# Optimization experiments

Measured on AMD Instinct MI355X. Metric: run time of the kernel, lower is better.

Reference implementation:

```python
import jax, jax.numpy as jnp
import numpy as np

N = 100000   # nodes
E = 1600000  # edges
D = 128      # input = hidden channels
L = 4        # 1 + num_convs GIN layers
G = 512      # graphs in batch
BN_EPS = 1e-5


def setup_inputs() -> dict:
    key = jax.random.key(0)
    ks = jax.random.split(key, 10)
    s = 1.0 / np.sqrt(D)
    x = jax.random.normal(ks[0], (N, D), jnp.float32)
    edge_index = jax.random.randint(ks[1], (2, E), 0, N)
    batch = jnp.sort(jax.random.randint(ks[2], (N,), 0, G))
    return {
        "x": x,
        "edge_index": edge_index,
        "batch": batch,
        "W1": jax.random.normal(ks[3], (L, D, D), jnp.float32) * s,
        "b1": jnp.zeros((L, D), jnp.float32),
        "gamma": jnp.ones((L, D), jnp.float32),
        "beta": jnp.zeros((L, D), jnp.float32),
        "W2": jax.random.normal(ks[4], (L, D, D), jnp.float32) * s,
        "b2": jnp.zeros((L, D), jnp.float32),
        "lin_W": jax.random.normal(ks[5], (D, 2), jnp.float32) * s,
        "lin_b": jnp.zeros((2,), jnp.float32),
    }


def reference(x, edge_index, batch, W1, b1, gamma, beta, W2, b2, lin_W, lin_b):
    src, dst = edge_index[0], edge_index[1]
    h = x
    for l in range(L):
        # GINConv, eps=0: (1+eps)*x_i + sum_{j->i} x_j  (scatter-add over edges)
        agg = jax.ops.segment_sum(h[src], dst, num_segments=N)  # [N, D]
        z = h + agg
        # MLP: Linear -> BatchNorm1d (training stats) -> ELU -> Linear -> ELU
        z = z @ W1[l] + b1[l]
        mu = jnp.mean(z, axis=0)
        var = jnp.mean((z - mu) ** 2, axis=0)  # biased var, as torch BN
        z = (z - mu) * jax.lax.rsqrt(var + BN_EPS) * gamma[l] + beta[l]
        z = jax.nn.elu(z)
        h = jax.nn.elu(z @ W2[l] + b2[l])
    # global_mean_pool: per-graph segment mean
    sums = jax.ops.segment_sum(h, batch, num_segments=G)             # [G, D]
    cnt = jax.ops.segment_sum(jnp.ones((N, 1), h.dtype), batch, num_segments=G)
    pooled = sums / jnp.maximum(cnt, 1.0)
    return pooled @ lin_W + lin_b  # [G, 2]
```

## Files before the change

kernel.cpp:

```cpp
#include <hip/hip_runtime.h>
#include <cstdint>

#define D 128
#define BKT_SHIFT 8
#define BKT_CAP 5120
#define EDGES_PER_BLOCK 4096
#define NREP 8

typedef __attribute__((ext_vector_type(4))) float floatx4;
typedef __attribute__((ext_vector_type(4))) _Float16 half4;
typedef __attribute__((ext_vector_type(8))) _Float16 half8;

__device__ __forceinline__ float elu_f(float x) {
    return x > 0.0f ? x : __expf(x) - 1.0f;
}

__global__ void init_cursor_kernel(int* __restrict__ gcursor, int NB) {
    int t = blockIdx.x * 256 + threadIdx.x;
    if (t < NB) gcursor[t] = t * BKT_CAP;
}

__global__ __launch_bounds__(256) void bucket_scatter_kernel(
    const int* __restrict__ src, const int* __restrict__ dst,
    int* __restrict__ gcursor, int2* __restrict__ staging, int E, int NB) {
    __shared__ int lcnt[512];
    __shared__ int lbase[512];
    int t = threadIdx.x;
    lcnt[t] = 0; lcnt[t + 256] = 0;
    __syncthreads();
    int base = blockIdx.x * EDGES_PER_BLOCK;
    int s_[16], d_[16], r_[16];
#pragma unroll
    for (int i = 0; i < 16; ++i) {
        int idx = base + i * 256 + t;
        if (idx < E) {
            s_[i] = src[idx];
            d_[i] = dst[idx];
            r_[i] = atomicAdd(&lcnt[d_[i] >> BKT_SHIFT], 1);
        }
    }
    __syncthreads();
    for (int b = t; b < NB; b += 256) {
        int c = lcnt[b];
        if (c) lbase[b] = atomicAdd(&gcursor[b], c);
    }
    __syncthreads();
#pragma unroll
    for (int i = 0; i < 16; ++i) {
        int idx = base + i * 256 + t;
        if (idx < E) {
            int bkt = d_[i] >> BKT_SHIFT;
            staging[lbase[bkt] + r_[i]] = make_int2(s_[i], d_[i]);
        }
    }
}

__global__ __launch_bounds__(256) void bucket_build_kernel(
    const int2* __restrict__ staging, const int* __restrict__ gcursor,
    int* __restrict__ rowstart, int* __restrict__ rowend,
    int* __restrict__ col, int N) {
    __shared__ int hcnt[256];
    __shared__ int hoff[256];
    int t = threadIdx.x;
    int node0 = blockIdx.x << BKT_SHIFT;
    int off0 = blockIdx.x * BKT_CAP;
    int off1 = gcursor[blockIdx.x];
    hcnt[t] = 0;
    __syncthreads();
    for (int i = off0 + t; i < off1; i += 256)
        atomicAdd(&hcnt[staging[i].y - node0], 1);
    __syncthreads();
    int deg = hcnt[t];
    hoff[t] = deg;
    __syncthreads();
    for (int off = 1; off < 256; off <<= 1) {
        int u = (t >= off) ? hoff[t - off] : 0;
        __syncthreads();
        hoff[t] += u;
        __syncthreads();
    }
    int myoff = (t == 0) ? 0 : hoff[t - 1];
    __syncthreads();
    hoff[t] = myoff;
    hcnt[t] = 0;
    if (node0 + t < N) {
        rowstart[node0 + t] = off0 + myoff;
        rowend[node0 + t] = off0 + myoff + deg;
    }
    __syncthreads();
    for (int i = off0 + t; i < off1; i += 256) {
        int2 p = staging[i];
        int dl = p.y - node0;
        int pos = off0 + hoff[dl] + atomicAdd(&hcnt[dl], 1);
        col[pos] = p.x;
    }
}

__global__ void to_half_kernel(const float* __restrict__ in, _Float16* __restrict__ outp, int n4) {
    int i = blockIdx.x * 256 + threadIdx.x;
    if (i >= n4) return;
    float4 v = ((const float4*)in)[i];
    half4 h = {(_Float16)v.x, (_Float16)v.y, (_Float16)v.z, (_Float16)v.w};
    ((half4*)outp)[i] = h;
}

__global__ void wprep_kernel(const float* __restrict__ W1, const float* __restrict__ W2,
                             _Float16* __restrict__ Wph, _Float16* __restrict__ Wpl,
                             int total) {
    int idx = blockIdx.x * 256 + threadIdx.x;
    if (idx >= total) return;
    int mat = idx >> 14;
    int rem = idx & 16383;
    int tile = rem >> 9;
    int lane = (rem >> 3) & 63;
    int j = rem & 7;
    int ks = tile >> 3, nt = tile & 7;
    int n = nt * 16 + (lane & 15);
    int k = ks * 32 + (lane >> 4) * 8 + j;
    int l = mat >> 1;
    const float* W = (mat & 1) ? W2 : W1;
    float v = W[(size_t)l * D * D + k * D + n];
    _Float16 h = (_Float16)v;
    _Float16 lo = (_Float16)(v - (float)h);
    Wph[idx] = h;
    Wpl[idx] = lo;
}

template <bool GATHER, bool ELU_OUT, bool STATS>
__global__ __launch_bounds__(256, 8) void gemm_mfma(
    const _Float16* __restrict__ Hh,
    const int* __restrict__ rowstart, const int* __restrict__ rowend,
    const int* __restrict__ col,
    const _Float16* __restrict__ Z,
    const _Float16* __restrict__ Wph, const _Float16* __restrict__ Wpl,
    const float* __restrict__ bias,
    const float* __restrict__ colsum_in, const float* __restrict__ gamma,
    const float* __restrict__ beta,
    _Float16* __restrict__ outp16, float* __restrict__ colsum_out, int N) {
    __shared__ _Float16 sA[64 * 136];
    __shared__ float bnsum[2 * D];
    __shared__ float s_sc[D];
    __shared__ float s_sh[D];
    const int tid = threadIdx.x;
    const int row0 = blockIdx.x * 64;

    if (STATS && tid < 2 * D) bnsum[tid] = 0.f;

    if (GATHER) {
        const int rg = tid >> 4;
        const int q = tid & 15;
        const half8* hh8 = (const half8*)Hh;
#pragma unroll
        for (int i = 0; i < 4; ++i) {
            int r = rg * 4 + i;
            int node = row0 + r;
            float a0 = 0.f, a1 = 0.f, a2 = 0.f, a3 = 0.f;
            float a4 = 0.f, a5 = 0.f, a6 = 0.f, a7 = 0.f;
            if (node < N) {
                half8 sf = hh8[(size_t)node * 16 + q];
                a0 = (float)sf[0]; a1 = (float)sf[1]; a2 = (float)sf[2]; a3 = (float)sf[3];
                a4 = (float)sf[4]; a5 = (float)sf[5]; a6 = (float)sf[6]; a7 = (float)sf[7];
                int e0 = rowstart[node], e1 = rowend[node];
                int e = e0;
                for (; e + 7 < e1; e += 8) {
                    int j0 = col[e],     j1 = col[e + 1], j2 = col[e + 2], j3 = col[e + 3];
                    int j4 = col[e + 4], j5 = col[e + 5], j6 = col[e + 6], j7 = col[e + 7];
                    half8 v0 = hh8[(size_t)j0 * 16 + q];
                    half8 v1 = hh8[(size_t)j1 * 16 + q];
                    half8 v2 = hh8[(size_t)j2 * 16 + q];
                    half8 v3 = hh8[(size_t)j3 * 16 + q];
                    half8 v4 = hh8[(size_t)j4 * 16 + q];
                    half8 v5 = hh8[(size_t)j5 * 16 + q];
                    half8 v6 = hh8[(size_t)j6 * 16 + q];
                    half8 v7 = hh8[(size_t)j7 * 16 + q];
                    a0 += ((float)v0[0] + (float)v1[0] + (float)v2[0] + (float)v3[0])
                        + ((float)v4[0] + (float)v5[0] + (float)v6[0] + (float)v7[0]);
                    a1 += ((float)v0[1] + (float)v1[1] + (float)v2[1] + (float)v3[1])
                        + ((float)v4[1] + (float)v5[1] + (float)v6[1] + (float)v7[1]);
                    a2 += ((float)v0[2] + (float)v1[2] + (float)v2[2] + (float)v3[2])
                        + ((float)v4[2] + (float)v5[2] + (float)v6[2] + (float)v7[2]);
                    a3 += ((float)v0[3] + (float)v1[3] + (float)v2[3] + (float)v3[3])
                        + ((float)v4[3] + (float)v5[3] + (float)v6[3] + (float)v7[3]);
                    a4 += ((float)v0[4] + (float)v1[4] + (float)v2[4] + (float)v3[4])
                        + ((float)v4[4] + (float)v5[4] + (float)v6[4] + (float)v7[4]);
                    a5 += ((float)v0[5] + (float)v1[5] + (float)v2[5] + (float)v3[5])
                        + ((float)v4[5] + (float)v5[5] + (float)v6[5] + (float)v7[5]);
                    a6 += ((float)v0[6] + (float)v1[6] + (float)v2[6] + (float)v3[6])
                        + ((float)v4[6] + (float)v5[6] + (float)v6[6] + (float)v7[6]);
                    a7 += ((float)v0[7] + (float)v1[7] + (float)v2[7] + (float)v3[7])
                        + ((float)v4[7] + (float)v5[7] + (float)v6[7] + (float)v7[7]);
                }
                for (; e < e1; ++e) {
                    half8 v = hh8[(size_t)col[e] * 16 + q];
                    a0 += (float)v[0]; a1 += (float)v[1]; a2 += (float)v[2]; a3 += (float)v[3];
                    a4 += (float)v[4]; a5 += (float)v[5]; a6 += (float)v[6]; a7 += (float)v[7];
                }
            }
            half8 hv = {(_Float16)a0, (_Float16)a1, (_Float16)a2, (_Float16)a3,
                        (_Float16)a4, (_Float16)a5, (_Float16)a6, (_Float16)a7};
            *(half8*)&sA[r * 136 + q * 8] = hv;
        }
    } else {
        if (tid < D) {
            float s = 0.f, s2 = 0.f;
#pragma unroll
            for (int rp = 0; rp < NREP; ++rp) {
                s  += colsum_in[rp * 2 * D + tid];
                s2 += colsum_in[rp * 2 * D + D + tid];
            }
            float invN = 1.0f / (float)N;
            float mu = s * invN;
            float var = s2 * invN - mu * mu;
            float rs = rsqrtf(var + 1e-5f);
            float sc = gamma[tid] * rs;
            s_sc[tid] = sc;
            s_sh[tid] = beta[tid] - mu * sc;
        }
        __syncthreads();
#pragma unroll
        for (int it = 0; it < 4; ++it) {
            int idx = tid + it * 256;
            int r = idx >> 4;
            int q8 = (idx & 15) * 8;
            int gr = row0 + r;
            half8 z = {};
            if (gr < N) z = *(const half8*)&Z[(size_t)gr * D + q8];
            float v0 = elu_f((float)z[0] * s_sc[q8 + 0] + s_sh[q8 + 0]);
            float v1 = elu_f((float)z[1] * s_sc[q8 + 1] + s_sh[q8 + 1]);
            float v2 = elu_f((float)z[2] * s_sc[q8 + 2] + s_sh[q8 + 2]);
            float v3 = elu_f((float)z[3] * s_sc[q8 + 3] + s_sh[q8 + 3]);
            float v4 = elu_f((float)z[4] * s_sc[q8 + 4] + s_sh[q8 + 4]);
            float v5 = elu_f((float)z[5] * s_sc[q8 + 5] + s_sh[q8 + 5]);
            float v6 = elu_f((float)z[6] * s_sc[q8 + 6] + s_sh[q8 + 6]);
            float v7 = elu_f((float)z[7] * s_sc[q8 + 7] + s_sh[q8 + 7]);
            half8 hv = {(_Float16)v0, (_Float16)v1, (_Float16)v2, (_Float16)v3,
                        (_Float16)v4, (_Float16)v5, (_Float16)v6, (_Float16)v7};
            *(half8*)&sA[r * 136 + q8] = hv;
        }
    }
    __syncthreads();

    const int wave = tid >> 6, lane = tid & 63;
    const int wm = wave >> 1, wn = wave & 1;
    const int l15 = lane & 15, quad = lane >> 4;
    const half8* bph = (const half8*)Wph;
    const half8* bpl = (const half8*)Wpl;

    floatx4 acc[2][4];
#pragma unroll
    for (int mt = 0; mt < 2; ++mt)
#pragma unroll
        for (int nt = 0; nt < 4; ++nt)
            acc[mt][nt] = (floatx4){0.f, 0.f, 0.f, 0.f};

#pragma unroll
    for (int ks = 0; ks < 4; ++ks) {
        const int kf = ks * 32 + quad * 8;
        half8 ah[2];
#pragma unroll
        for (int mt = 0; mt < 2; ++mt)
            ah[mt] = *(const half8*)&sA[(wm * 32 + mt * 16 + l15) * 136 + kf];
#pragma unroll
        for (int nt = 0; nt < 4; ++nt) {
            int tIdx = (ks * 8 + wn * 4 + nt) * 64 + lane;
            half8 bh = bph[tIdx];
            half8 bl = bpl[tIdx];
            acc[0][nt] = __builtin_amdgcn_mfma_f32_16x16x32_f16(ah[0], bh, acc[0][nt], 0, 0, 0);
            acc[1][nt] = __builtin_amdgcn_mfma_f32_16x16x32_f16(ah[1], bh, acc[1][nt], 0, 0, 0);
            acc[0][nt] = __builtin_amdgcn_mfma_f32_16x16x32_f16(ah[0], bl, acc[0][nt], 0, 0, 0);
            acc[1][nt] = __builtin_amdgcn_mfma_f32_16x16x32_f16(ah[1], bl, acc[1][nt], 0, 0, 0);
        }
    }

#pragma unroll
    for (int nt = 0; nt < 4; ++nt) {
        int c = wn * 64 + nt * 16 + l15;
        float b = bias[c];
        float s = 0.f, s2 = 0.f;
#pragma unroll
        for (int mt = 0; mt < 2; ++mt) {
#pragma unroll
            for (int r = 0; r < 4; ++r) {
                int gm = row0 + wm * 32 + mt * 16 + quad * 4 + r;
                float v = acc[mt][nt][r] + b;
                if (ELU_OUT) v = elu_f(v);
                if (gm < N) {
                    outp16[(size_t)gm * D + c] = (_Float16)v;
                    if (STATS) { s += v; s2 += v * v; }
                }
            }
        }
        if (STATS) {
            atomicAdd(&bnsum[c], s);
            atomicAdd(&bnsum[D + c], s2);
        }
    }
    if (STATS) {
        __syncthreads();
        float* rep = colsum_out + (size_t)(blockIdx.x & (NREP - 1)) * 2 * D;
        if (tid < D) {
            atomicAdd(&rep[tid], bnsum[tid]);
            atomicAdd(&rep[D + tid], bnsum[D + tid]);
        }
    }
}

__global__ __launch_bounds__(128) void pool_kernel(
    const _Float16* __restrict__ h, const int* __restrict__ batch,
    float* __restrict__ pooled, float* __restrict__ cnt, int N) {
    int c = threadIdx.x;
    int r0 = blockIdx.x * 256;
    if (r0 >= N) return;
    int rend = r0 + 256; if (rend > N) rend = N;
    int cur = batch[r0];
    float acc = 0.f;
    float cacc = 0.f;
    for (int r = r0; r < rend; ++r) {
        int b = batch[r];
        if (b != cur) {
            atomicAdd(&pooled[(size_t)cur * D + c], acc);
            if (c == 0) atomicAdd(&cnt[cur], cacc);
            acc = 0.f; cacc = 0.f; cur = b;
        }
        acc += (float)h[(size_t)r * D + c];
        cacc += 1.f;
    }
    atomicAdd(&pooled[(size_t)cur * D + c], acc);
    if (c == 0) atomicAdd(&cnt[cur], cacc);
}

__global__ void final_linear_kernel(const float* __restrict__ pooled,
                                    const float* __restrict__ cnt,
                                    const float* __restrict__ linW,
                                    const float* __restrict__ linb,
                                    float* __restrict__ out, int G) {
    int t = blockIdx.x * blockDim.x + threadIdx.x;
    if (t >= G * 2) return;
    int g = t >> 1, o = t & 1;
    float inv = 1.0f / fmaxf(cnt[g], 1.0f);
    float s = linb[o];
    for (int c = 0; c < D; ++c)
        s += pooled[(size_t)g * D + c] * inv * linW[c * 2 + o];
    out[t] = s;
}

extern "C" void kernel_launch(void* const* d_in, const int* in_sizes, int n_in,
                              void* d_out, int out_size, void* d_ws, size_t ws_size,
                              hipStream_t stream) {
    const float* x      = (const float*)d_in[0];
    const int*  eidx    = (const int*)d_in[1];
    const int*  batch   = (const int*)d_in[2];
    const float* W1     = (const float*)d_in[3];
    const float* b1     = (const float*)d_in[4];
    const float* gamma  = (const float*)d_in[5];
    const float* beta   = (const float*)d_in[6];
    const float* W2     = (const float*)d_in[7];
    const float* b2     = (const float*)d_in[8];
    const float* linW   = (const float*)d_in[9];
    const float* linb   = (const float*)d_in[10];
    float* out = (float*)d_out;

    const int N = in_sizes[0] / D;
    const int E = in_sizes[1] / 2;
    const int L = in_sizes[3] / (D * D);
    const int G = out_size / 2;
    const int* esrc = eidx;
    const int* edst = eidx + E;
    const int NB = (N + 255) >> 8;

    size_t off = 0;
    auto carve = [&](size_t bytes) -> void* {
        void* p = (char*)d_ws + off;
        off += (bytes + 255) & ~(size_t)255;
        return p;
    };
    const size_t ND = (size_t)N * D;
    const int WTOT = 2 * L * D * D;
    _Float16* z16   = (_Float16*)carve(ND * 2);
    _Float16* hhalf = (_Float16*)carve(ND * 2);
    _Float16* Wph = (_Float16*)carve((size_t)WTOT * 2);
    _Float16* Wpl = (_Float16*)carve((size_t)WTOT * 2);
    int* rowstart = (int*)carve((size_t)N * 4);
    int* rowend   = (int*)carve((size_t)N * 4);
    int* col      = (int*)carve((size_t)NB * BKT_CAP * 4);
    float* colsum4 = (float*)carve((size_t)4 * NREP * 2 * D * 4);
    int* gcursor  = (int*)carve(512 * 4);
    float* pooled = (float*)carve((size_t)G * D * 4);
    float* cnt    = (float*)carve((size_t)G * 4);
    int2* staging = (int2*)z16;
    (void)ws_size; (void)n_in;

    hipMemsetAsync(colsum4, 0, (size_t)4 * NREP * 2 * D * 4, stream);
    hipMemsetAsync(pooled, 0, (size_t)G * D * 4 + (size_t)G * 4, stream);

    const int EB = (E + EDGES_PER_BLOCK - 1) / EDGES_PER_BLOCK;
    init_cursor_kernel<<<(NB + 255) / 256, 256, 0, stream>>>(gcursor, NB);
    bucket_scatter_kernel<<<EB, 256, 0, stream>>>(esrc, edst, gcursor, staging, E, NB);
    bucket_build_kernel<<<NB, 256, 0, stream>>>(staging, gcursor, rowstart, rowend, col, N);
    wprep_kernel<<<(WTOT + 255) / 256, 256, 0, stream>>>(W1, W2, Wph, Wpl, WTOT);
    to_half_kernel<<<(int)((ND / 4 + 255) / 256), 256, 0, stream>>>(x, hhalf, (int)(ND / 4));

    const int gemm_grid = (N + 63) / 64;
    for (int l = 0; l < L; ++l) {
        float* colsum = colsum4 + (size_t)l * NREP * 2 * D;
        gemm_mfma<true, false, true><<<gemm_grid, 256, 0, stream>>>(
            hhalf, rowstart, rowend, col, nullptr,
            Wph + (size_t)(l * 2) * D * D, Wpl + (size_t)(l * 2) * D * D,
            b1 + (size_t)l * D, nullptr, nullptr, nullptr, z16, colsum, N);
        gemm_mfma<false, true, false><<<gemm_grid, 256, 0, stream>>>(
            nullptr, nullptr, nullptr, nullptr, z16,
            Wph + (size_t)(l * 2 + 1) * D * D, Wpl + (size_t)(l * 2 + 1) * D * D,
            b2 + (size_t)l * D, colsum, gamma + (size_t)l * D, beta + (size_t)l * D,
            hhalf, nullptr, N);
    }

    pool_kernel<<<(N + 255) / 256, 128, 0, stream>>>(hhalf, batch, pooled, cnt, N);
    final_linear_kernel<<<(G * 2 + 255) / 256, 256, 0, stream>>>(pooled, cnt, linW, linb, out, G);
}
```

Measured before the change: 668.1 us.

## Halve GEMM row tile to 32 and gather with 32 lanes of half4 per row

Cuts the fused gather+GEMM row tile from 64 to 32 nodes per block, which doubles the grid, and has each wave compute one 16-row MFMA tile instead of two. The neighbor gather now uses 32 threads per node, each loading half4, in place of 16 threads loading half8. This gives more independent gather streams and narrower per-thread work, and uses 32-bit index arithmetic. The intent is more parallelism and latency hiding for the irregular gather. The cost is more blocks, smaller loads per thread, and less reuse of the weight fragments per block.

Measured after the change: 741.0 us. 1.11x slower.

```diff
diff --git a/kernel.cpp b/kernel.cpp
--- a/kernel.cpp
+++ b/kernel.cpp
@@ -137,42 +137,40 @@
     const float* __restrict__ colsum_in, const float* __restrict__ gamma,
     const float* __restrict__ beta,
     _Float16* __restrict__ outp16, float* __restrict__ colsum_out, int N) {
-    __shared__ _Float16 sA[64 * 136];
+    __shared__ _Float16 sA[32 * 136];
     __shared__ float bnsum[2 * D];
     __shared__ float s_sc[D];
     __shared__ float s_sh[D];
     const int tid = threadIdx.x;
-    const int row0 = blockIdx.x * 64;
+    const int row0 = blockIdx.x * 32;
 
     if (STATS && tid < 2 * D) bnsum[tid] = 0.f;
 
     if (GATHER) {
-        const int rg = tid >> 4;
-        const int q = tid & 15;
-        const half8* hh8 = (const half8*)Hh;
+        const int rg = tid >> 5;
+        const int q = tid & 31;
+        const half4* hh4 = (const half4*)Hh;
 #pragma unroll
         for (int i = 0; i < 4; ++i) {
             int r = rg * 4 + i;
             int node = row0 + r;
             float a0 = 0.f, a1 = 0.f, a2 = 0.f, a3 = 0.f;
-            float a4 = 0.f, a5 = 0.f, a6 = 0.f, a7 = 0.f;
             if (node < N) {
-                half8 sf = hh8[(size_t)node * 16 + q];
+                half4 sf = hh4[(uint32_t)(node * 32 + q)];
                 a0 = (float)sf[0]; a1 = (float)sf[1]; a2 = (float)sf[2]; a3 = (float)sf[3];
-                a4 = (float)sf[4]; a5 = (float)sf[5]; a6 = (float)sf[6]; a7 = (float)sf[7];
                 int e0 = rowstart[node], e1 = rowend[node];
                 int e = e0;
                 for (; e + 7 < e1; e += 8) {
                     int j0 = col[e],     j1 = col[e + 1], j2 = col[e + 2], j3 = col[e + 3];
                     int j4 = col[e + 4], j5 = col[e + 5], j6 = col[e + 6], j7 = col[e + 7];
-                    half8 v0 = hh8[(size_t)j0 * 16 + q];
-                    half8 v1 = hh8[(size_t)j1 * 16 + q];
-                    half8 v2 = hh8[(size_t)j2 * 16 + q];
-                    half8 v3 = hh8[(size_t)j3 * 16 + q];
-                    half8 v4 = hh8[(size_t)j4 * 16 + q];
-                    half8 v5 = hh8[(size_t)j5 * 16 + q];
-                    half8 v6 = hh8[(size_t)j6 * 16 + q];
-                    half8 v7 = hh8[(size_t)j7 * 16 + q];
+                    half4 v0 = hh4[(uint32_t)(j0 * 32 + q)];
+                    half4 v1 = hh4[(uint32_t)(j1 * 32 + q)];
+                    half4 v2 = hh4[(uint32_t)(j2 * 32 + q)];
+                    half4 v3 = hh4[(uint32_t)(j3 * 32 + q)];
+                    half4 v4 = hh4[(uint32_t)(j4 * 32 + q)];
+                    half4 v5 = hh4[(uint32_t)(j5 * 32 + q)];
+                    half4 v6 = hh4[(uint32_t)(j6 * 32 + q)];
+                    half4 v7 = hh4[(uint32_t)(j7 * 32 + q)];
                     a0 += ((float)v0[0] + (float)v1[0] + (float)v2[0] + (float)v3[0])
                         + ((float)v4[0] + (float)v5[0] + (float)v6[0] + (float)v7[0]);
                     a1 += ((float)v0[1] + (float)v1[1] + (float)v2[1] + (float)v3[1])
@@ -181,24 +179,14 @@
                         + ((float)v4[2] + (float)v5[2] + (float)v6[2] + (float)v7[2]);
                     a3 += ((float)v0[3] + (float)v1[3] + (float)v2[3] + (float)v3[3])
                         + ((float)v4[3] + (float)v5[3] + (float)v6[3] + (float)v7[3]);
-                    a4 += ((float)v0[4] + (float)v1[4] + (float)v2[4] + (float)v3[4])
-                        + ((float)v4[4] + (float)v5[4] + (float)v6[4] + (float)v7[4]);
-                    a5 += ((float)v0[5] + (float)v1[5] + (float)v2[5] + (float)v3[5])
-                        + ((float)v4[5] + (float)v5[5] + (float)v6[5] + (float)v7[5]);
-                    a6 += ((float)v0[6] + (float)v1[6] + (float)v2[6] + (float)v3[6])
-                        + ((float)v4[6] + (float)v5[6] + (float)v6[6] + (float)v7[6]);
-                    a7 += ((float)v0[7] + (float)v1[7] + (float)v2[7] + (float)v3[7])
-                        + ((float)v4[7] + (float)v5[7] + (float)v6[7] + (float)v7[7]);
                 }
                 for (; e < e1; ++e) {
-                    half8 v = hh8[(size_t)col[e] * 16 + q];
+                    half4 v = hh4[(uint32_t)(col[e] * 32 + q)];
                     a0 += (float)v[0]; a1 += (float)v[1]; a2 += (float)v[2]; a3 += (float)v[3];
-                    a4 += (float)v[4]; a5 += (float)v[5]; a6 += (float)v[6]; a7 += (float)v[7];
                 }
             }
-            half8 hv = {(_Float16)a0, (_Float16)a1, (_Float16)a2, (_Float16)a3,
-                        (_Float16)a4, (_Float16)a5, (_Float16)a6, (_Float16)a7};
-            *(half8*)&sA[r * 136 + q * 8] = hv;
+            half4 hv = {(_Float16)a0, (_Float16)a1, (_Float16)a2, (_Float16)a3};
+            *(half4*)&sA[r * 136 + q * 4] = hv;
         }
     } else {
         if (tid < D) {
@@ -218,7 +206,7 @@
         }
         __syncthreads();
 #pragma unroll
-        for (int it = 0; it < 4; ++it) {
+        for (int it = 0; it < 2; ++it) {
             int idx = tid + it * 256;
             int r = idx >> 4;
             int q8 = (idx & 15) * 8;
@@ -246,29 +234,22 @@
     const half8* bph = (const half8*)Wph;
     const half8* bpl = (const half8*)Wpl;
 
-    floatx4 acc[2][4];
-#pragma unroll
-    for (int mt = 0; mt < 2; ++mt)
-#pragma unroll
-        for (int nt = 0; nt < 4; ++nt)
-            acc[mt][nt] = (floatx4){0.f, 0.f, 0.f, 0.f};
+    floatx4 acc[4];
+#pragma unroll
+    for (int nt = 0; nt < 4; ++nt)
+        acc[nt] = (floatx4){0.f, 0.f, 0.f, 0.f};
 
 #pragma unroll
     for (int ks = 0; ks < 4; ++ks) {
         const int kf = ks * 32 + quad * 8;
-        half8 ah[2];
-#pragma unroll
-        for (int mt = 0; mt < 2; ++mt)
-            ah[mt] = *(const half8*)&sA[(wm * 32 + mt * 16 + l15) * 136 + kf];
+        half8 ah = *(const half8*)&sA[(wm * 16 + l15) * 136 + kf];
 #pragma unroll
         for (int nt = 0; nt < 4; ++nt) {
             int tIdx = (ks * 8 + wn * 4 + nt) * 64 + lane;
             half8 bh = bph[tIdx];
             half8 bl = bpl[tIdx];
-            acc[0][nt] = __builtin_amdgcn_mfma_f32_16x16x32_f16(ah[0], bh, acc[0][nt], 0, 0, 0);
-            acc[1][nt] = __builtin_amdgcn_mfma_f32_16x16x32_f16(ah[1], bh, acc[1][nt], 0, 0, 0);
-            acc[0][nt] = __builtin_amdgcn_mfma_f32_16x16x32_f16(ah[0], bl, acc[0][nt], 0, 0, 0);
-            acc[1][nt] = __builtin_amdgcn_mfma_f32_16x16x32_f16(ah[1], bl, acc[1][nt], 0, 0, 0);
+            acc[nt] = __builtin_amdgcn_mfma_f32_16x16x32_f16(ah, bh, acc[nt], 0, 0, 0);
+            acc[nt] = __builtin_amdgcn_mfma_f32_16x16x32_f16(ah, bl, acc[nt], 0, 0, 0);
         }
     }
 
@@ -278,16 +259,13 @@
         float b = bias[c];
         float s = 0.f, s2 = 0.f;
 #pragma unroll
-        for (int mt = 0; mt < 2; ++mt) {
-#pragma unroll
-            for (int r = 0; r < 4; ++r) {
-                int gm = row0 + wm * 32 + mt * 16 + quad * 4 + r;
-                float v = acc[mt][nt][r] + b;
-                if (ELU_OUT) v = elu_f(v);
-                if (gm < N) {
-                    outp16[(size_t)gm * D + c] = (_Float16)v;
-                    if (STATS) { s += v; s2 += v * v; }
-                }
+        for (int r = 0; r < 4; ++r) {
+            int gm = row0 + wm * 16 + quad * 4 + r;
+            float v = acc[nt][r] + b;
+            if (ELU_OUT) v = elu_f(v);
+            if (gm < N) {
+                outp16[(size_t)gm * D + c] = (_Float16)v;
+                if (STATS) { s += v; s2 += v * v; }
             }
         }
         if (STATS) {
@@ -400,7 +378,7 @@
     wprep_kernel<<<(WTOT + 255) / 256, 256, 0, stream>>>(W1, W2, Wph, Wpl, WTOT);
     to_half_kernel<<<(int)((ND / 4 + 255) / 256), 256, 0, stream>>>(x, hhalf, (int)(ND / 4));
 
-    const int gemm_grid = (N + 63) / 64;
+    const int gemm_grid = (N + 31) / 32;
     for (int l = 0; l < L; ++l) {
         float* colsum = colsum4 + (size_t)l * NREP * 2 * D;
         gemm_mfma<true, false, true><<<gemm_grid, 256, 0, stream>>>(
```
